# Performance work log

Measured on AMD Instinct MI355X. Metric: run time of the kernel, lower is better.

## Reference

```python
import jax, jax.numpy as jnp
import numpy as np

CAP = 15.0
EPS = 1e-6
NUM_HEADS = 16
HEAD_DIM = 64

def _rmsnorm(x, w):
    xf = x.astype(jnp.float32)
    var = jnp.mean(xf * xf, axis=-1, keepdims=True)
    return w * (xf * jax.lax.rsqrt(var + EPS)).astype(x.dtype)

def _gate(g):
    # sigmoid(soft_cap(g)) with cap 15
    return jax.nn.sigmoid(CAP * jnp.tanh(g / CAP))

def setup_inputs() -> dict:
    key = jax.random.key(0)
    ks = jax.random.split(key, 4)
    B, S, D = 4, 2048, 1024
    H, Dh = NUM_HEADS, HEAD_DIM
    return {
        "x": jax.random.normal(ks[0], (B, S, D), jnp.float32),
        "hidden_state": jnp.zeros((B, H, Dh, Dh), jnp.float32),
        "w_rms": jnp.ones((D,), jnp.float32),
        "w_qkv": jax.random.normal(ks[1], (D, 3 * H * Dh), jnp.float32) * 0.02,
        "w_gate": jax.random.normal(ks[2], (D, 3 * H), jnp.float32) * 0.02,
        "w_out": jax.random.normal(ks[3], (D, D), jnp.float32) * 0.02,
    }

def reference(x, hidden_state, w_rms, w_qkv, w_gate, w_out):
    B, S, D = x.shape
    H, Dh = NUM_HEADS, HEAD_DIM
    residual = x
    xn = _rmsnorm(x, w_rms)
    qkv = (xn @ w_qkv).reshape(B, S, 3, H, Dh)
    q, k, v = qkv[:, :, 0], qkv[:, :, 1], qkv[:, :, 2]  # [B,S,H,Dh]
    gates = _gate((xn @ w_gate).reshape(B, S, 3, H))
    i_g, f_g, o_g = gates[:, :, 0], gates[:, :, 1], gates[:, :, 2]  # [B,S,H]

    # time-major for scan: [S,B,H,...]
    def tm(a):
        return jnp.moveaxis(a, 1, 0)

    def step(state, inp):
        qt, kt, vt, it, ft, ot = inp  # [B,H,Dh]/[B,H]
        kv = kt[..., :, None] * vt[..., None, :]            # [B,H,Dh,Dh]
        state = ft[..., None, None] * state + it[..., None, None] * kv
        h = jnp.einsum('bhd,bhde->bhe', qt, state) * ot[..., None]
        return state, h

    _, h_seq = jax.lax.scan(step, hidden_state,
                            (tm(q), tm(k), tm(v), tm(i_g), tm(f_g), tm(o_g)))
    out = jnp.moveaxis(h_seq, 0, 1).reshape(B, S, H * Dh) @ w_out
    return residual + out
```

## Files before the change

### kernel.cpp

```cpp
#include <hip/hip_runtime.h>
#include <math.h>

typedef unsigned short u16;
typedef unsigned int   u32;
typedef __bf16 bf16x8 __attribute__((ext_vector_type(8)));
typedef float  f32x4  __attribute__((ext_vector_type(4)));

#define NBATCH 4
#define SEQ    2048
#define DIM    1024
#define NH     16
#define BH     64
#define NC     32
#define ROWS   8192
#define N1     3200

__device__ __forceinline__ u16 f2bf(float f) {
  u32 u = __builtin_bit_cast(u32, f);
  u32 r = u + 0x7fffu + ((u >> 16) & 1u);
  return (u16)(r >> 16);
}
__device__ __forceinline__ float bf2f(u16 h) {
  return __builtin_bit_cast(float, (u32)h << 16);
}

__device__ __forceinline__ void gl2lds16(const u16* g, u16* l) {
  __builtin_amdgcn_global_load_lds(
      (const __attribute__((address_space(1))) u32*)g,
      (__attribute__((address_space(3))) u32*)l, 16, 0, 0);
}

__global__ __launch_bounds__(256) void transpose_w(const float* __restrict__ W,
                                                   u16* __restrict__ Bt, int K, int N) {
  __shared__ float tile[32][33];
  const int n0 = blockIdx.x * 32, k0 = blockIdx.y * 32;
  const int tx = threadIdx.x, ty = threadIdx.y;
  #pragma unroll
  for (int i = 0; i < 4; i++)
    tile[ty + i * 8][tx] = W[(size_t)(k0 + ty + i * 8) * N + n0 + tx];
  __syncthreads();
  #pragma unroll
  for (int i = 0; i < 4; i++)
    Bt[(size_t)(n0 + ty + i * 8) * K + k0 + tx] = f2bf(tile[tx][ty + i * 8]);
}

__global__ __launch_bounds__(256) void fill_gateW(const float* __restrict__ wg,
                                                  u16* __restrict__ Bt) {
  const int g = blockIdx.x;
  const int tid = threadIdx.x;
  #pragma unroll
  for (int kk = 0; kk < 4; kk++) {
    const int k = kk * 256 + tid;
    u16 v = 0;
    if (g < 48) v = f2bf(wg[(size_t)k * 48 + g]);
    Bt[(size_t)(3072 + g) * 1024 + k] = v;
  }
}

__global__ __launch_bounds__(256) void rmsnorm_k(const float* __restrict__ x,
                                                 const float* __restrict__ w,
                                                 u16* __restrict__ xn) {
  const int row = blockIdx.x, tid = threadIdx.x;
  const float4 xv = *(const float4*)&x[(size_t)row * 1024 + tid * 4];
  float ss = xv.x * xv.x + xv.y * xv.y + xv.z * xv.z + xv.w * xv.w;
  #pragma unroll
  for (int off = 32; off > 0; off >>= 1) ss += __shfl_down(ss, off);
  __shared__ float red[4];
  if ((tid & 63) == 0) red[tid >> 6] = ss;
  __syncthreads();
  const float tot = red[0] + red[1] + red[2] + red[3];
  const float scale = rsqrtf(tot * (1.0f / 1024.0f) + 1e-6f);
  const float4 wv = *(const float4*)&w[tid * 4];
  const u16 o0 = f2bf(xv.x * scale * wv.x), o1 = f2bf(xv.y * scale * wv.y);
  const u16 o2 = f2bf(xv.z * scale * wv.z), o3 = f2bf(xv.w * scale * wv.w);
  uint2 ov;
  ov.x = (u32)o0 | ((u32)o1 << 16);
  ov.y = (u32)o2 | ((u32)o3 << 16);
  *(uint2*)&xn[(size_t)row * 1024 + tid * 4] = ov;
}

__device__ __forceinline__ void gemm_core256(const u16* __restrict__ A, const u16* __restrict__ Bt,
                                             int K, int rowBase, int colBase,
                                             u16* As, u16* Bs, f32x4 (&acc)[4][4]) {
  const int tid = threadIdx.x;
  const int lane = tid & 63;
  const int q = lane >> 4, m16 = lane & 15;
  const int wave = tid >> 6;
  const int wm = wave & 3, wn = wave >> 2;
  const int cA0 = tid;
  const int cA1 = tid + 512;
  const int cB  = tid;
  const u16* gA0 = &A [(size_t)(rowBase + (cA0 >> 2)) * K + (cA0 & 3) * 8];
  const u16* gA1 = &A [(size_t)(rowBase + (cA1 >> 2)) * K + (cA1 & 3) * 8];
  const u16* gB  = &Bt[(size_t)(colBase + (cB  >> 2)) * K + (cB  & 3) * 8];
  u16* lA0 = As + cA0 * 8;
  u16* lA1 = As + cA1 * 8;
  u16* lB  = Bs + cB * 8;
  for (int kb = 0; kb < K / 32; ++kb) {
    __syncthreads();
    gl2lds16(gA0, lA0);
    gl2lds16(gA1, lA1);
    gl2lds16(gB,  lB);
    gA0 += 32; gA1 += 32; gB += 32;
    __syncthreads();
    bf16x8 af[4], bfr[4];
    #pragma unroll
    for (int mi = 0; mi < 4; mi++)
      af[mi] = *(const bf16x8*)&As[(wm * 64 + mi * 16 + m16) * 32 + q * 8];
    #pragma unroll
    for (int ni = 0; ni < 4; ni++)
      bfr[ni] = *(const bf16x8*)&Bs[(wn * 64 + ni * 16 + m16) * 32 + q * 8];
    #pragma unroll
    for (int mi = 0; mi < 4; mi++)
      #pragma unroll
      for (int ni = 0; ni < 4; ni++)
        acc[mi][ni] = __builtin_amdgcn_mfma_f32_16x16x32_bf16(af[mi], bfr[ni], acc[mi][ni], 0, 0, 0);
  }
}

__global__ __launch_bounds__(512, 4) void gemm_qkv(const u16* __restrict__ A, const u16* __restrict__ Bt,
                                                   u16* __restrict__ Qb, u16* __restrict__ Kb,
                                                   u16* __restrict__ Vb, float* __restrict__ gates) {
  __shared__ __attribute__((aligned(16))) u16 As[256 * 32];
  __shared__ __attribute__((aligned(16))) u16 Bs[128 * 32];
  f32x4 acc[4][4] = {};
  const int rowBase = blockIdx.x * 256, colBase = blockIdx.y * 128;
  gemm_core256(A, Bt, 1024, rowBase, colBase, As, Bs, acc);
  const int tid = threadIdx.x;
  const int lane = tid & 63, wave = tid >> 6;
  const int q = lane >> 4, m16 = lane & 15;
  const int wm = wave & 3, wn = wave >> 2;
  __syncthreads();
  if (colBase < 3072) {
    const int which = colBase >> 10;
    u16* dstBase = (which == 0) ? Qb : ((which == 1) ? Kb : Vb);
    const int b = rowBase >> 11;
    const int h = ((colBase & 1023) >> 6) + wn;
    const int tRow0 = (rowBase & 2047) + wm * 64;
    u16* scratch = As + wave * 1024;
    u16* headBase = dstBase + ((size_t)(b * 16 + h)) * 2048 * 64;
    const int rr = lane >> 2, co = (lane & 3) * 16;
    #pragma unroll
    for (int mi = 0; mi < 4; mi++) {
      #pragma unroll
      for (int ni = 0; ni < 4; ni++)
        #pragma unroll
        for (int r = 0; r < 4; r++)
          scratch[(q * 4 + r) * 64 + ni * 16 + m16] = f2bf(acc[mi][ni][r]);
      const uint4 d0 = *(const uint4*)&scratch[rr * 64 + co];
      const uint4 d1 = *(const uint4*)&scratch[rr * 64 + co + 8];
      u16* gp = headBase + (size_t)(tRow0 + mi * 16 + rr) * 64 + co;
      *(uint4*)gp = d0;
      *(uint4*)(gp + 8) = d1;
    }
  } else {
    #pragma unroll
    for (int ni = 0; ni < 4; ni++) {
      const int c2 = wn * 64 + ni * 16 + m16;
      if (c2 < 48) {
        const int which = c2 >> 4, hh = c2 & 15;
        #pragma unroll
        for (int mi = 0; mi < 4; mi++)
          #pragma unroll
          for (int r = 0; r < 4; r++) {
            const int grow = rowBase + wm * 64 + mi * 16 + q * 4 + r;
            const int b = grow >> 11, t = grow & 2047;
            const float v = acc[mi][ni][r];
            const float g = 1.0f / (1.0f + expf(-(15.0f * tanhf(v * (1.0f / 15.0f)))));
            gates[((size_t)which * 64 + (b * 16 + hh)) * 2048 + t] = g;
          }
      }
    }
  }
}

__global__ __launch_bounds__(512, 4) void gemm_out(const u16* __restrict__ A, const u16* __restrict__ Bt,
                                                   const float* __restrict__ resid,
                                                   float* __restrict__ out) {
  __shared__ __attribute__((aligned(16))) u16 As[256 * 32];
  __shared__ __attribute__((aligned(16))) u16 Bs[128 * 32];
  f32x4 acc[4][4] = {};
  const int rowBase = blockIdx.x * 256, colBase = blockIdx.y * 128;
  gemm_core256(A, Bt, 1024, rowBase, colBase, As, Bs, acc);
  const int tid = threadIdx.x;
  const int lane = tid & 63, wave = tid >> 6;
  const int q = lane >> 4, m16 = lane & 15;
  const int wm = wave & 3, wn = wave >> 2;
  #pragma unroll
  for (int mi = 0; mi < 4; mi++)
    #pragma unroll
    for (int ni = 0; ni < 4; ni++)
      #pragma unroll
      for (int r = 0; r < 4; r++) {
        const int grow = rowBase + wm * 64 + mi * 16 + q * 4 + r;
        const int gcol = colBase + wn * 64 + ni * 16 + m16;
        const size_t idx = (size_t)grow * 1024 + gcol;
        out[idx] = acc[mi][ni][r] + resid[idx];
      }
}

__global__ __launch_bounds__(64) void la_k(const float* __restrict__ gates,
                                           float* __restrict__ la) {
  const int bh = blockIdx.x >> 5, c = blockIdx.x & 31, lane = threadIdx.x;
  const int t = c * 64 + lane;
  float x = logf(gates[(size_t)(64 + bh) * 2048 + t]);
  #pragma unroll
  for (int off = 1; off < 64; off <<= 1) {
    const float y = __shfl_up(x, off);
    if (lane >= off) x += y;
  }
  la[(size_t)bh * 2048 + t] = x;
}

__global__ __launch_bounds__(256) void passA_k(const u16* __restrict__ Qb, const u16* __restrict__ Kb,
                                               const u16* __restrict__ Vb,
                                               const float* __restrict__ gates,
                                               const float* __restrict__ la,
                                               float* __restrict__ Mbuf, u16* __restrict__ hseq) {
  __shared__ u16 Ql[64][72], Kl[64][72], KTl[64][72], VTl[64][72], Pl[64][72];
  __shared__ float laS[64], iS[64];
  const int tid = threadIdx.x;
  const int bh = blockIdx.x >> 5, c = blockIdx.x & 31;
  const int lane = tid & 63, w = tid >> 6;
  const int q = lane >> 4, m16 = lane & 15;
  const size_t base = ((size_t)bh * 2048 + c * 64) * 64;
  const int tbase = bh * 2048 + c * 64;

  {
    const int s = tid >> 2, db = (tid & 3) * 16;
    if (tid < 64) {
      laS[tid] = la[tbase + tid];
      iS[tid] = gates[(size_t)bh * 2048 + c * 64 + tid];
    }
    const float la_s = la[tbase + s];
    const float i_s = gates[(size_t)bh * 2048 + c * 64 + s];
    const float la63 = la[tbase + 63];
    const float wk = expf(la63 - la_s) * i_s;
    const uint4 q0 = *(const uint4*)&Qb[base + s * 64 + db];
    const uint4 q1 = *(const uint4*)&Qb[base + s * 64 + db + 8];
    *(uint4*)&Ql[s][db] = q0;
    *(uint4*)&Ql[s][db + 8] = q1;
    const uint4 k0 = *(const uint4*)&Kb[base + s * 64 + db];
    const uint4 k1 = *(const uint4*)&Kb[base + s * 64 + db + 8];
    *(uint4*)&Kl[s][db] = k0;
    *(uint4*)&Kl[s][db + 8] = k1;
    u16 ktmp[16];
    *(uint4*)&ktmp[0] = k0;
    *(uint4*)&ktmp[8] = k1;
    #pragma unroll
    for (int j = 0; j < 16; j++) KTl[db + j][s] = f2bf(wk * bf2f(ktmp[j]));
    const uint4 v0 = *(const uint4*)&Vb[base + s * 64 + db];
    const uint4 v1 = *(const uint4*)&Vb[base + s * 64 + db + 8];
    u16 vtmp[16];
    *(uint4*)&vtmp[0] = v0;
    *(uint4*)&vtmp[8] = v1;
    #pragma unroll
    for (int j = 0; j < 16; j++) VTl[db + j][s] = vtmp[j];
  }
  __syncthreads();

  f32x4 pacc[4] = {};
  #pragma unroll
  for (int ks = 0; ks < 2; ks++) {
    const bf16x8 aq = *(const bf16x8*)&Ql[w * 16 + m16][ks * 32 + q * 8];
    #pragma unroll
    for (int ni = 0; ni < 4; ni++) {
      const bf16x8 bk = *(const bf16x8*)&Kl[ni * 16 + m16][ks * 32 + q * 8];
      pacc[ni] = __builtin_amdgcn_mfma_f32_16x16x32_bf16(aq, bk, pacc[ni], 0, 0, 0);
    }
  }
  #pragma unroll
  for (int ni = 0; ni < 4; ni++)
    #pragma unroll
    for (int r = 0; r < 4; r++) {
      const int tt = w * 16 + q * 4 + r, ss = ni * 16 + m16;
      float Wts = 0.0f;
      if (ss <= tt) Wts = expf(laS[tt] - laS[ss]) * iS[ss];
      Pl[tt][ss] = f2bf(pacc[ni][r] * Wts);
    }
  __syncthreads();

  f32x4 hacc[4] = {}, macc[4] = {};
  #pragma unroll
  for (int ks = 0; ks < 2; ks++) {
    const bf16x8 ap = *(const bf16x8*)&Pl[w * 16 + m16][ks * 32 + q * 8];
    const bf16x8 ak = *(const bf16x8*)&KTl[w * 16 + m16][ks * 32 + q * 8];
    #pragma unroll
    for (int ni = 0; ni < 4; ni++) {
      const bf16x8 bv = *(const bf16x8*)&VTl[ni * 16 + m16][ks * 32 + q * 8];
      hacc[ni] = __builtin_amdgcn_mfma_f32_16x16x32_bf16(ap, bv, hacc[ni], 0, 0, 0);
      macc[ni] = __builtin_amdgcn_mfma_f32_16x16x32_bf16(ak, bv, macc[ni], 0, 0, 0);
    }
  }
  const int b = bh >> 4, h = bh & 15;
  #pragma unroll
  for (int ni = 0; ni < 4; ni++)
    #pragma unroll
    for (int r = 0; r < 4; r++) {
      const int tt = w * 16 + q * 4 + r, e = ni * 16 + m16;
      const int tg = c * 64 + tt;
      hseq[((size_t)b * 2048 + tg) * 1024 + h * 64 + e] = f2bf(hacc[ni][r]);
      Mbuf[(((size_t)bh * 32 + c) * 64 + tt) * 64 + e] = macc[ni][r];
    }
}

__global__ __launch_bounds__(256) void passB_k(float* __restrict__ Mbuf,
                                               const float* __restrict__ hidden,
                                               const float* __restrict__ la) {
  const int bh = blockIdx.x >> 4;
  const int e = (blockIdx.x & 15) * 256 + threadIdx.x;
  __shared__ float Gs[32];
  if (threadIdx.x < 32)
    Gs[threadIdx.x] = expf(la[(size_t)bh * 2048 + threadIdx.x * 64 + 63]);
  __syncthreads();
  float st = hidden[(size_t)bh * 4096 + e];
  float* M = &Mbuf[(size_t)bh * 32 * 4096 + e];
  float m_next = M[0];
  #pragma unroll 4
  for (int c = 0; c < 32; c++) {
    const float m_cur = m_next;
    if (c < 31) m_next = M[(size_t)(c + 1) * 4096];
    M[(size_t)c * 4096] = st;
    st = Gs[c] * st + m_cur;
  }
}

__global__ __launch_bounds__(256) void passC_k(const u16* __restrict__ Qb,
                                               const float* __restrict__ Sprev,
                                               const float* __restrict__ la,
                                               const float* __restrict__ gates,
                                               u16* __restrict__ hseq) {
  __shared__ u16 aQl[64][72], STl[64][72];
  const int tid = threadIdx.x;
  const int bh = blockIdx.x >> 5, c = blockIdx.x & 31;
  const int lane = tid & 63, w = tid >> 6;
  const int q = lane >> 4, m16 = lane & 15;
  const size_t base = ((size_t)bh * 2048 + c * 64) * 64;
  const int tbase = bh * 2048 + c * 64;
  {
    const int s = tid >> 2, db = (tid & 3) * 16;
    const float a_s = expf(la[tbase + s]);
    const uint4 q0 = *(const uint4*)&Qb[base + s * 64 + db];
    const uint4 q1 = *(const uint4*)&Qb[base + s * 64 + db + 8];
    u16 qtmp[16];
    *(uint4*)&qtmp[0] = q0;
    *(uint4*)&qtmp[8] = q1;
    #pragma unroll
    for (int j = 0; j < 16; j++) aQl[s][db + j] = f2bf(a_s * bf2f(qtmp[j]));
    const float* Sp = &Sprev[((size_t)bh * 32 + c) * 4096];
    #pragma unroll
    for (int j = 0; j < 16; j++) STl[db + j][s] = f2bf(Sp[s * 64 + db + j]);
  }
  __syncthreads();
  f32x4 acc[4] = {};
  #pragma unroll
  for (int ks = 0; ks < 2; ks++) {
    const bf16x8 a = *(const bf16x8*)&aQl[w * 16 + m16][ks * 32 + q * 8];
    #pragma unroll
    for (int ni = 0; ni < 4; ni++) {
      const bf16x8 bb = *(const bf16x8*)&STl[ni * 16 + m16][ks * 32 + q * 8];
      acc[ni] = __builtin_amdgcn_mfma_f32_16x16x32_bf16(a, bb, acc[ni], 0, 0, 0);
    }
  }
  const int b = bh >> 4, h = bh & 15;
  #pragma unroll
  for (int ni = 0; ni < 4; ni++)
    #pragma unroll
    for (int r = 0; r < 4; r++) {
      const int tt = w * 16 + q * 4 + r, e = ni * 16 + m16;
      const int tg = c * 64 + tt;
      const float o = gates[(size_t)(128 + bh) * 2048 + tg];
      const size_t idx = ((size_t)b * 2048 + tg) * 1024 + h * 64 + e;
      hseq[idx] = f2bf(o * (bf2f(hseq[idx]) + acc[ni][r]));
    }
}

extern "C" void kernel_launch(void* const* d_in, const int* in_sizes, int n_in,
                              void* d_out, int out_size, void* d_ws, size_t ws_size,
                              hipStream_t stream) {
  (void)in_sizes; (void)n_in; (void)out_size; (void)ws_size;
  const float* x      = (const float*)d_in[0];
  const float* hidden = (const float*)d_in[1];
  const float* w_rms  = (const float*)d_in[2];
  const float* w_qkv  = (const float*)d_in[3];
  const float* w_gate = (const float*)d_in[4];
  const float* w_out  = (const float*)d_in[5];
  float* out = (float*)d_out;

  char* p = (char*)d_ws;
  u16* wqkvT = (u16*)p;  p += (size_t)N1 * 1024 * 2;
  u16* woutT = (u16*)p;  p += (size_t)1024 * 1024 * 2;
  u16* xn    = (u16*)p;  p += (size_t)ROWS * 1024 * 2;
  u16* Qb    = (u16*)p;  p += (size_t)BH * 2048 * 64 * 2;
  u16* Kb    = (u16*)p;  p += (size_t)BH * 2048 * 64 * 2;
  u16* Vb    = (u16*)p;  p += (size_t)BH * 2048 * 64 * 2;
  float* gates = (float*)p; p += (size_t)3 * BH * 2048 * 4;
  float* la    = (float*)p; p += (size_t)BH * 2048 * 4;
  float* Mbuf  = (float*)p; p += (size_t)BH * NC * 4096 * 4;
  u16* hseq  = (u16*)p;  p += (size_t)ROWS * 1024 * 2;

  transpose_w<<<dim3(96, 32), dim3(32, 8), 0, stream>>>(w_qkv, wqkvT, 1024, 3072);
  transpose_w<<<dim3(32, 32), dim3(32, 8), 0, stream>>>(w_out, woutT, 1024, 1024);
  fill_gateW<<<128, 256, 0, stream>>>(w_gate, wqkvT);
  rmsnorm_k<<<ROWS, 256, 0, stream>>>(x, w_rms, xn);
  gemm_qkv<<<dim3(32, 25), 512, 0, stream>>>(xn, wqkvT, Qb, Kb, Vb, gates);
  la_k<<<BH * NC, 64, 0, stream>>>(gates, la);
  passA_k<<<BH * NC, 256, 0, stream>>>(Qb, Kb, Vb, gates, la, Mbuf, hseq);
  passB_k<<<BH * 16, 256, 0, stream>>>(Mbuf, hidden, la);
  passC_k<<<BH * NC, 256, 0, stream>>>(Qb, Mbuf, la, gates, hseq);
  gemm_out<<<dim3(32, 8), 512, 0, stream>>>(hseq, woutT, x, out);
}
```

Baseline: 272.0 us.

## Fuse log-gate prefix scan into passA and retile output GEMM to 128x128

Removes the separate la_k launch by computing the per-chunk cumulative log forget gate inside passA_k, which writes it to shared memory and to global memory for the later passes. The output GEMM moves from 256x128 tiles with 512 threads to 128x128 tiles with 256 threads, doubling the grid to 512 blocks so more of the CUs are filled. The cost is an extra sync in passA, and the smaller GEMM tiles reuse loaded data less.

```diff
diff --git a/kernel.cpp b/kernel.cpp
--- a/kernel.cpp
+++ b/kernel.cpp
@@ -118,6 +118,47 @@
   }
 }
 
+__device__ __forceinline__ void gemm_core128(const u16* __restrict__ A, const u16* __restrict__ Bt,
+                                             int K, int rowBase, int colBase,
+                                             u16* As, u16* Bs, f32x4 (&acc)[4][4]) {
+  const int tid = threadIdx.x;
+  const int lane = tid & 63;
+  const int q = lane >> 4, m16 = lane & 15;
+  const int wave = tid >> 6;
+  const int wm = wave & 1, wn = wave >> 1;
+  const int srow = wave * 16 + (lane >> 2);
+  const int scol = (lane & 3) * 8;
+  const u16* gA0 = &A [(size_t)(rowBase + srow) * K + scol];
+  const u16* gA1 = gA0 + (size_t)64 * K;
+  const u16* gB0 = &Bt[(size_t)(colBase + srow) * K + scol];
+  const u16* gB1 = gB0 + (size_t)64 * K;
+  u16* lA0 = As + wave * 512 + lane * 8;
+  u16* lA1 = lA0 + 2048;
+  u16* lB0 = Bs + wave * 512 + lane * 8;
+  u16* lB1 = lB0 + 2048;
+  for (int kb = 0; kb < K / 32; ++kb) {
+    __syncthreads();
+    gl2lds16(gA0, lA0);
+    gl2lds16(gA1, lA1);
+    gl2lds16(gB0, lB0);
+    gl2lds16(gB1, lB1);
+    gA0 += 32; gA1 += 32; gB0 += 32; gB1 += 32;
+    __syncthreads();
+    bf16x8 af[4], bfr[4];
+    #pragma unroll
+    for (int mi = 0; mi < 4; mi++)
+      af[mi] = *(const bf16x8*)&As[(wm * 64 + mi * 16 + m16) * 32 + q * 8];
+    #pragma unroll
+    for (int ni = 0; ni < 4; ni++)
+      bfr[ni] = *(const bf16x8*)&Bs[(wn * 64 + ni * 16 + m16) * 32 + q * 8];
+    #pragma unroll
+    for (int mi = 0; mi < 4; mi++)
+      #pragma unroll
+      for (int ni = 0; ni < 4; ni++)
+        acc[mi][ni] = __builtin_amdgcn_mfma_f32_16x16x32_bf16(af[mi], bfr[ni], acc[mi][ni], 0, 0, 0);
+  }
+}
+
 __global__ __launch_bounds__(512, 4) void gemm_qkv(const u16* __restrict__ A, const u16* __restrict__ Bt,
                                                    u16* __restrict__ Qb, u16* __restrict__ Kb,
                                                    u16* __restrict__ Vb, float* __restrict__ gates) {
@@ -174,18 +215,18 @@
   }
 }
 
-__global__ __launch_bounds__(512, 4) void gemm_out(const u16* __restrict__ A, const u16* __restrict__ Bt,
+__global__ __launch_bounds__(256, 4) void gemm_out(const u16* __restrict__ A, const u16* __restrict__ Bt,
                                                    const float* __restrict__ resid,
                                                    float* __restrict__ out) {
-  __shared__ __attribute__((aligned(16))) u16 As[256 * 32];
+  __shared__ __attribute__((aligned(16))) u16 As[128 * 32];
   __shared__ __attribute__((aligned(16))) u16 Bs[128 * 32];
   f32x4 acc[4][4] = {};
-  const int rowBase = blockIdx.x * 256, colBase = blockIdx.y * 128;
-  gemm_core256(A, Bt, 1024, rowBase, colBase, As, Bs, acc);
+  const int rowBase = blockIdx.x * 128, colBase = blockIdx.y * 128;
+  gemm_core128(A, Bt, 1024, rowBase, colBase, As, Bs, acc);
   const int tid = threadIdx.x;
   const int lane = tid & 63, wave = tid >> 6;
   const int q = lane >> 4, m16 = lane & 15;
-  const int wm = wave & 3, wn = wave >> 2;
+  const int wm = wave & 1, wn = wave >> 1;
   #pragma unroll
   for (int mi = 0; mi < 4; mi++)
     #pragma unroll
@@ -199,23 +240,10 @@
       }
 }
 
-__global__ __launch_bounds__(64) void la_k(const float* __restrict__ gates,
-                                           float* __restrict__ la) {
-  const int bh = blockIdx.x >> 5, c = blockIdx.x & 31, lane = threadIdx.x;
-  const int t = c * 64 + lane;
-  float x = logf(gates[(size_t)(64 + bh) * 2048 + t]);
-  #pragma unroll
-  for (int off = 1; off < 64; off <<= 1) {
-    const float y = __shfl_up(x, off);
-    if (lane >= off) x += y;
-  }
-  la[(size_t)bh * 2048 + t] = x;
-}
-
 __global__ __launch_bounds__(256) void passA_k(const u16* __restrict__ Qb, const u16* __restrict__ Kb,
                                                const u16* __restrict__ Vb,
                                                const float* __restrict__ gates,
-                                               const float* __restrict__ la,
+                                               float* __restrict__ la,
                                                float* __restrict__ Mbuf, u16* __restrict__ hseq) {
   __shared__ u16 Ql[64][72], Kl[64][72], KTl[64][72], VTl[64][72], Pl[64][72];
   __shared__ float laS[64], iS[64];
@@ -224,18 +252,24 @@
   const int lane = tid & 63, w = tid >> 6;
   const int q = lane >> 4, m16 = lane & 15;
   const size_t base = ((size_t)bh * 2048 + c * 64) * 64;
-  const int tbase = bh * 2048 + c * 64;
+  const int toff = c * 64;
+
+  if (tid < 64) {
+    float lg = logf(gates[(size_t)(64 + bh) * 2048 + toff + tid]);
+    #pragma unroll
+    for (int off = 1; off < 64; off <<= 1) {
+      const float y = __shfl_up(lg, off);
+      if (tid >= off) lg += y;
+    }
+    laS[tid] = lg;
+    iS[tid] = gates[(size_t)bh * 2048 + toff + tid];
+    la[(size_t)bh * 2048 + toff + tid] = lg;
+  }
+  __syncthreads();
 
   {
     const int s = tid >> 2, db = (tid & 3) * 16;
-    if (tid < 64) {
-      laS[tid] = la[tbase + tid];
-      iS[tid] = gates[(size_t)bh * 2048 + c * 64 + tid];
-    }
-    const float la_s = la[tbase + s];
-    const float i_s = gates[(size_t)bh * 2048 + c * 64 + s];
-    const float la63 = la[tbase + 63];
-    const float wk = expf(la63 - la_s) * i_s;
+    const float wk = expf(laS[63] - laS[s]) * iS[s];
     const uint4 q0 = *(const uint4*)&Qb[base + s * 64 + db];
     const uint4 q1 = *(const uint4*)&Qb[base + s * 64 + db + 8];
     *(uint4*)&Ql[s][db] = q0;
@@ -404,9 +438,8 @@
   fill_gateW<<<128, 256, 0, stream>>>(w_gate, wqkvT);
   rmsnorm_k<<<ROWS, 256, 0, stream>>>(x, w_rms, xn);
   gemm_qkv<<<dim3(32, 25), 512, 0, stream>>>(xn, wqkvT, Qb, Kb, Vb, gates);
-  la_k<<<BH * NC, 64, 0, stream>>>(gates, la);
   passA_k<<<BH * NC, 256, 0, stream>>>(Qb, Kb, Vb, gates, la, Mbuf, hseq);
   passB_k<<<BH * 16, 256, 0, stream>>>(Mbuf, hidden, la);
   passC_k<<<BH * NC, 256, 0, stream>>>(Qb, Mbuf, la, gates, hseq);
-  gemm_out<<<dim3(32, 8), 512, 0, stream>>>(hseq, woutT, x, out);
-}
+  gemm_out<<<dim3(64, 8), 256, 0, stream>>>(hseq, woutT, x, out);
+}
```

New measurement: 269.2 us. Within noise of the previous version (-1.1%).
